# Optimization experiments

Measured on AMD Instinct MI355X. Metric: run time of the kernel, lower is better.

## Reference

```python
import jax, jax.numpy as jnp
import numpy as np

K = 5  # top-k neighbors (init kwarg k)
EPS = 1e-12

def _normalize(x):
    n = jnp.linalg.norm(x, axis=1, keepdims=True)
    return x / jnp.maximum(n, EPS)

def setup_inputs() -> dict:
    key = jax.random.key(0)
    k1, k2, k3 = jax.random.split(key, 3)
    B, D, N, C = 1024, 1024, 100000, 1000
    features = jax.random.normal(k1, (B, D), dtype=jnp.float32)
    idx = jax.random.randint(k2, (B,), 0, N, dtype=jnp.int64)
    # buffers: feat_memory = F.normalize(rand(N, D)); pred_memory = ones(N, C)/C
    feat_memory = _normalize(jax.random.uniform(k3, (N, D), dtype=jnp.float32))
    pred_memory = jnp.ones((N, C), dtype=jnp.float32) / C
    return {"features": features, "idx": idx,
            "feat_memory": feat_memory, "pred_memory": pred_memory}

def reference(features, idx, feat_memory, pred_memory):
    B = features.shape[0]
    x = _normalize(features)                       # [B, D]
    dis = x @ feat_memory.T                        # [B, N] similarity
    # self-mask: each row's own bank entry set to global min (min is invariant
    # under this assignment, so the per-row torch loop vectorizes exactly)
    m = jnp.min(dis)
    dis = dis.at[jnp.arange(B), idx].set(m)
    _, indices = jax.lax.top_k(dis, K)             # [B, K]
    mean_logits = jnp.mean(pred_memory[indices], axis=1)  # [B, C]
    pseudo_labels = jnp.argmax(mean_logits, axis=1)       # [B]
    return pseudo_labels, mean_logits
```

## Files before the change

### kernel.cpp

```cpp
#include <hip/hip_runtime.h>
#include <stdint.h>
#include <stddef.h>

#define B_ROWS 1024
#define D_DIM  1024
#define N_MEM  100000
#define C_CLS  1000
#define K_TOP  5

#define BM 256
#define BN 256
#define BKT 64
#define NKT (D_DIM / BKT)
#define NT_TILES ((N_MEM + BN - 1) / BN)
#define NPAD (NT_TILES * BN)
#define BT_TILES (B_ROWS / BM)
#define NT_PER_XCD 49
#define GRID_GEMM (8 * NT_PER_XCD * BT_TILES)

typedef __bf16 bf16;
typedef bf16 bf16x4 __attribute__((ext_vector_type(4)));
typedef bf16 bf16x8 __attribute__((ext_vector_type(8)));
typedef float f32x4 __attribute__((ext_vector_type(4)));

#define MFMA16(a, b, c) __builtin_amdgcn_mfma_f32_16x16x32_bf16((a), (b), (c), 0, 0, 0)
#define BARRIER() do { asm volatile("" ::: "memory"); \
                       __builtin_amdgcn_s_barrier();  \
                       asm volatile("" ::: "memory"); } while (0)
#define WAITVM(N) asm volatile("s_waitcnt vmcnt(" #N ")" ::: "memory")

__device__ __forceinline__ void insert5(float v, int n, float tv[K_TOP], int ti[K_TOP]) {
#pragma unroll
  for (int j = 0; j < K_TOP; ++j) {
    bool gt = v > tv[j];
    float ov = tv[j]; int oi = ti[j];
    tv[j] = gt ? v : ov;  ti[j] = gt ? n : oi;
    v = gt ? ov : v;      n = gt ? oi : n;
  }
}

__global__ __launch_bounds__(256) void k_normalize(const float* __restrict__ F,
                                                   bf16* __restrict__ X) {
  int row = blockIdx.x;
  int tid = threadIdx.x;
  const float4* fr = (const float4*)(F + (size_t)row * D_DIM);
  float4 v = fr[tid];
  float s = v.x * v.x + v.y * v.y + v.z * v.z + v.w * v.w;
  for (int off = 32; off > 0; off >>= 1) s += __shfl_down(s, off, 64);
  __shared__ float wred[4];
  if ((tid & 63) == 0) wred[tid >> 6] = s;
  __syncthreads();
  float tot = wred[0] + wred[1] + wred[2] + wred[3];
  float inv = 1.0f / fmaxf(sqrtf(tot), 1e-12f);
  bf16x4 o;
  o[0] = (bf16)(v.x * inv);
  o[1] = (bf16)(v.y * inv);
  o[2] = (bf16)(v.z * inv);
  o[3] = (bf16)(v.w * inv);
  *(bf16x4*)(X + (size_t)row * D_DIM + (size_t)tid * 4) = o;
}

__global__ __launch_bounds__(256) void k_convert(const float* __restrict__ FM,
                                                 bf16* __restrict__ FMB,
                                                 int total8, int pad8) {
  int i = blockIdx.x * 256 + threadIdx.x;
  if (i >= pad8) return;
  bf16x8 o;
  if (i < total8) {
    float4 a = ((const float4*)FM)[2 * i];
    float4 b = ((const float4*)FM)[2 * i + 1];
    o[0] = (bf16)a.x; o[1] = (bf16)a.y; o[2] = (bf16)a.z; o[3] = (bf16)a.w;
    o[4] = (bf16)b.x; o[5] = (bf16)b.y; o[6] = (bf16)b.z; o[7] = (bf16)b.w;
  } else {
#pragma unroll
    for (int e = 0; e < 8; ++e) o[e] = (bf16)0.f;
  }
  ((bf16x8*)FMB)[i] = o;
}

__device__ __forceinline__ void gl_lds16(const bf16* g, char* l) {
  __builtin_amdgcn_global_load_lds((__attribute__((address_space(1))) void*)g,
                                   (__attribute__((address_space(3))) void*)l,
                                   16, 0, 0);
}

#define STAGE_HALF(g, off, rbase, k0) do {                                     \
    gl_lds16((g) + (size_t)(rbase) * D_DIM + (k0),      lds + (off) + d0);     \
    gl_lds16((g) + (size_t)((rbase) + 64) * D_DIM + (k0), lds + (off) + d1);   \
  } while (0)

__global__ __launch_bounds__(512, 2) void k_gemm_topk(const bf16* __restrict__ X,
                                                      const bf16* __restrict__ FMB,
                                                      const int* __restrict__ IDX,
                                                      float2* __restrict__ CAND) {
  extern __shared__ char lds[];
  int bid = blockIdx.x;
  int xcd = bid & 7;
  int jj = bid >> 3;
  int cnt = (xcd < 7) ? NT_PER_XCD : (NT_TILES - 7 * NT_PER_XCD);
  if (jj >= 4 * cnt) return;
  int nt = xcd * NT_PER_XCD + (jj >> 2);
  int bt = jj & 3;
  size_t row0 = (size_t)bt * BM;
  size_t col0 = (size_t)nt * BN;

  int tid = threadIdx.x;
  int lane = tid & 63;
  int wv = tid >> 6;
  int wm = wv >> 2, wn = wv & 3;
  int frow = lane & 15, q = lane >> 4;
  int cs0 = ((q ^ (frow & 7)) * 16);
  int cs1 = (((q + 4) ^ (frow & 7)) * 16);

  int arow0 = tid >> 3;
  int jsrc = (tid & 7) ^ (arow0 & 7);
  const bf16* gA = X   + ((size_t)row0 + arow0) * D_DIM + jsrc * 8;
  const bf16* gB = FMB + ((size_t)col0 + arow0) * D_DIM + jsrc * 8;
  int d0 = tid * 16;
  int d1 = 8192 + tid * 16;

  STAGE_HALF(gA, 0,     0,   0);
  STAGE_HALF(gA, 16384, 128, 0);
  STAGE_HALF(gB, 32768, 0,   0);
  STAGE_HALF(gB, 49152, 128, 0);
  STAGE_HALF(gA, 65536 + 0,     0,   BKT);
  STAGE_HALF(gA, 65536 + 16384, 128, BKT);
  STAGE_HALF(gB, 65536 + 32768, 0,   BKT);
  STAGE_HALF(gB, 65536 + 49152, 128, BKT);

  f32x4 acc[8][4];
#pragma unroll
  for (int mi = 0; mi < 8; ++mi)
#pragma unroll
    for (int ni = 0; ni < 4; ++ni)
      acc[mi][ni] = (f32x4){0.f, 0.f, 0.f, 0.f};

  WAITVM(8);
  BARRIER();

#pragma unroll 2
  for (int kt = 0; kt < NKT; ++kt) {
    char* buf = lds + ((kt & 1) << 16);
    const char* Ab = buf + wm * 16384 + frow * 128;
    const char* Bb = buf + 32768 + ((wn >> 1) * 16384) + ((wn & 1) * 8192) + frow * 128;
    int bufoff = (kt & 1) << 16;
    int k2 = (kt + 2) * BKT;
    bool do_stage = (kt < NKT - 2);
    bf16x8 af[4][2], bfr[4][2];

#pragma unroll
    for (int mi = 0; mi < 4; ++mi) {
      af[mi][0] = *(const bf16x8*)(Ab + mi * 2048 + cs0);
      af[mi][1] = *(const bf16x8*)(Ab + mi * 2048 + cs1);
    }
#pragma unroll
    for (int nb = 0; nb < 2; ++nb) {
      bfr[nb][0] = *(const bf16x8*)(Bb + nb * 2048 + cs0);
      bfr[nb][1] = *(const bf16x8*)(Bb + nb * 2048 + cs1);
    }
    BARRIER();
    __builtin_amdgcn_s_setprio(1);
#pragma unroll
    for (int mi = 0; mi < 4; ++mi)
#pragma unroll
      for (int nb = 0; nb < 2; ++nb) {
        acc[mi][nb] = MFMA16(af[mi][0], bfr[nb][0], acc[mi][nb]);
        acc[mi][nb] = MFMA16(af[mi][1], bfr[nb][1], acc[mi][nb]);
      }
    __builtin_amdgcn_s_setprio(0);
    BARRIER();

#pragma unroll
    for (int nb = 2; nb < 4; ++nb) {
      bfr[nb][0] = *(const bf16x8*)(Bb + nb * 2048 + cs0);
      bfr[nb][1] = *(const bf16x8*)(Bb + nb * 2048 + cs1);
    }
    BARRIER();
    __builtin_amdgcn_s_setprio(1);
#pragma unroll
    for (int mi = 0; mi < 4; ++mi)
#pragma unroll
      for (int nb = 2; nb < 4; ++nb) {
        acc[mi][nb] = MFMA16(af[mi][0], bfr[nb][0], acc[mi][nb]);
        acc[mi][nb] = MFMA16(af[mi][1], bfr[nb][1], acc[mi][nb]);
      }
    __builtin_amdgcn_s_setprio(0);
    BARRIER();

#pragma unroll
    for (int mi = 0; mi < 4; ++mi) {
      af[mi][0] = *(const bf16x8*)(Ab + 8192 + mi * 2048 + cs0);
      af[mi][1] = *(const bf16x8*)(Ab + 8192 + mi * 2048 + cs1);
    }
    if (do_stage) {
      STAGE_HALF(gB, bufoff + 32768, 0,   k2);
      STAGE_HALF(gB, bufoff + 49152, 128, k2);
    }
    BARRIER();
    __builtin_amdgcn_s_setprio(1);
#pragma unroll
    for (int mi = 0; mi < 4; ++mi)
#pragma unroll
      for (int nb = 2; nb < 4; ++nb) {
        acc[4 + mi][nb] = MFMA16(af[mi][0], bfr[nb][0], acc[4 + mi][nb]);
        acc[4 + mi][nb] = MFMA16(af[mi][1], bfr[nb][1], acc[4 + mi][nb]);
      }
    __builtin_amdgcn_s_setprio(0);
    BARRIER();

    if (do_stage) {
      STAGE_HALF(gA, bufoff + 0,     0,   k2);
      STAGE_HALF(gA, bufoff + 16384, 128, k2);
    }
    BARRIER();
    __builtin_amdgcn_s_setprio(1);
#pragma unroll
    for (int mi = 0; mi < 4; ++mi)
#pragma unroll
      for (int nb = 0; nb < 2; ++nb) {
        acc[4 + mi][nb] = MFMA16(af[mi][0], bfr[nb][0], acc[4 + mi][nb]);
        acc[4 + mi][nb] = MFMA16(af[mi][1], bfr[nb][1], acc[4 + mi][nb]);
      }
    __builtin_amdgcn_s_setprio(0);
    if (kt < NKT - 2) { WAITVM(8); } else { WAITVM(0); }
    BARRIER();
  }

  int Rbase = wm * 128 + q * 4;
#pragma unroll
  for (int mi = 0; mi < 8; ++mi)
#pragma unroll
    for (int ni = 0; ni < 4; ++ni) {
      int Cc = wn * 64 + ni * 16 + frow;
      int chunkC = Cc >> 3;
      int e2 = (Cc & 7) * 2;
#pragma unroll
      for (int r = 0; r < 4; ++r) {
        int R = Rbase + mi * 16 + r;
        *(bf16*)(lds + R * 512 + ((chunkC ^ (R & 31)) * 16) + e2) = (bf16)acc[mi][ni][r];
      }
    }
  __syncthreads();

  int tr = tid >> 1, h = tid & 1;
  int grow = (int)row0 + tr;
  int self = IDX[grow];
  float tv[K_TOP]; int ti[K_TOP];
#pragma unroll
  for (int j = 0; j < K_TOP; ++j) { tv[j] = -1e30f; ti[j] = -1; }
  int swz = tr & 31;
#pragma unroll
  for (int c8 = 0; c8 < 16; ++c8) {
    int chunk = h * 16 + c8;
    bf16x8 v8 = *(const bf16x8*)(lds + tr * 512 + ((chunk ^ swz) * 16));
#pragma unroll
    for (int e = 0; e < 8; ++e) {
      int gc = (int)col0 + chunk * 8 + e;
      if (gc >= N_MEM || gc == self) continue;
      float v = (float)v8[e];
      if (v > tv[K_TOP - 1]) insert5(v, gc, tv, ti);
    }
  }
  float pv[K_TOP]; int pi[K_TOP];
#pragma unroll
  for (int j = 0; j < K_TOP; ++j) {
    pv[j] = __shfl_xor(tv[j], 1, 64);
    pi[j] = __shfl_xor(ti[j], 1, 64);
  }
#pragma unroll
  for (int j = 0; j < K_TOP; ++j)
    if (pv[j] > tv[K_TOP - 1]) insert5(pv[j], pi[j], tv, ti);

  if (h == 0) {
    float2* out = CAND + ((size_t)grow * NT_TILES + nt) * K_TOP;
#pragma unroll
    for (int j = 0; j < K_TOP; ++j)
      out[j] = make_float2(tv[j], __int_as_float(ti[j]));
  }
}

__device__ void gather_mean_argmax(const int* find, const float* __restrict__ P,
                                   float* __restrict__ OUT, int b, int tid) {
  float bestV = -1e30f;
  int bestC = 0;
  for (int c = tid; c < C_CLS; c += 256) {
    float s = 0.f;
    for (int j = 0; j < K_TOP; ++j) s += P[(size_t)find[j] * C_CLS + c];
    float mean = s * (1.0f / K_TOP);
    OUT[(size_t)B_ROWS + (size_t)b * C_CLS + c] = mean;
    if (mean > bestV) { bestV = mean; bestC = c; }
  }
  __shared__ float rv[256];
  __shared__ int rc[256];
  rv[tid] = bestV; rc[tid] = bestC;
  for (int s = 128; s >= 1; s >>= 1) {
    __syncthreads();
    if (tid < s) {
      float v2 = rv[tid + s]; int c2 = rc[tid + s];
      if (v2 > rv[tid] || (v2 == rv[tid] && c2 < rc[tid])) { rv[tid] = v2; rc[tid] = c2; }
    }
  }
  __syncthreads();
  if (tid == 0) OUT[b] = (float)rc[0];
}

__global__ __launch_bounds__(256) void k_merge(const float2* __restrict__ CAND,
                                               const float* __restrict__ P,
                                               float* __restrict__ OUT) {
  int b = blockIdx.x;
  int tid = threadIdx.x;
  const float2* row = CAND + (size_t)b * (NT_TILES * K_TOP);

  float tv[K_TOP]; int ti[K_TOP];
  for (int j = 0; j < K_TOP; ++j) { tv[j] = -1e30f; ti[j] = -1; }
  for (int i = tid; i < NT_TILES * K_TOP; i += 256) {
    float2 e = row[i];
    float v = e.x;
    if (v > tv[K_TOP - 1]) insert5(v, __float_as_int(e.y), tv, ti);
  }

  __shared__ float sv[256 * K_TOP];
  __shared__ int si[256 * K_TOP];
  for (int j = 0; j < K_TOP; ++j) { sv[tid * K_TOP + j] = tv[j]; si[tid * K_TOP + j] = ti[j]; }
  for (int s = 128; s >= 1; s >>= 1) {
    __syncthreads();
    if (tid < s) {
      for (int j = 0; j < K_TOP; ++j) {
        float v = sv[(tid + s) * K_TOP + j];
        int n = si[(tid + s) * K_TOP + j];
        if (v > tv[K_TOP - 1]) insert5(v, n, tv, ti);
      }
      for (int j = 0; j < K_TOP; ++j) { sv[tid * K_TOP + j] = tv[j]; si[tid * K_TOP + j] = ti[j]; }
    }
  }
  __syncthreads();
  __shared__ int find[K_TOP];
  if (tid == 0)
    for (int j = 0; j < K_TOP; ++j) {
      int v = si[j];
      find[j] = (v < 0) ? 0 : (v >= N_MEM ? N_MEM - 1 : v);
    }
  __syncthreads();
  gather_mean_argmax(find, P, OUT, b, tid);
}

__global__ __launch_bounds__(256) void k_naive(const float* __restrict__ F,
                                               const int* __restrict__ IDX,
                                               const float* __restrict__ FM,
                                               const float* __restrict__ P,
                                               float* __restrict__ OUT) {
  int b = blockIdx.x;
  int tid = threadIdx.x;
  __shared__ float wred[4];
  const float4* fr = (const float4*)(F + (size_t)b * D_DIM);
  float4 v = fr[tid];
  float s = v.x * v.x + v.y * v.y + v.z * v.z + v.w * v.w;
  for (int off = 32; off > 0; off >>= 1) s += __shfl_down(s, off, 64);
  if ((tid & 63) == 0) wred[tid >> 6] = s;
  __syncthreads();
  float inv = 1.0f / fmaxf(sqrtf(wred[0] + wred[1] + wred[2] + wred[3]), 1e-12f);
  float4 xv = make_float4(v.x * inv, v.y * inv, v.z * inv, v.w * inv);
  __syncthreads();
  int self = IDX[b];
  __shared__ float ptv[K_TOP];
  __shared__ int pti[K_TOP];
  if (tid < K_TOP) { ptv[tid] = -1e30f; pti[tid] = 0; }
  __syncthreads();
  for (int n = 0; n < N_MEM; ++n) {
    const float4* frow = (const float4*)(FM + (size_t)n * D_DIM);
    float4 fv = frow[tid];
    float p = xv.x * fv.x + xv.y * fv.y + xv.z * fv.z + xv.w * fv.w;
    for (int off = 32; off > 0; off >>= 1) p += __shfl_down(p, off, 64);
    if ((tid & 63) == 0) wred[tid >> 6] = p;
    __syncthreads();
    if (tid == 0 && n != self) {
      float tot = wred[0] + wred[1] + wred[2] + wred[3];
      if (tot > ptv[K_TOP - 1]) {
        int q = K_TOP - 1;
        while (q > 0 && tot > ptv[q - 1]) { ptv[q] = ptv[q - 1]; pti[q] = pti[q - 1]; --q; }
        ptv[q] = tot; pti[q] = n;
      }
    }
    __syncthreads();
  }
  __shared__ int find[K_TOP];
  if (tid < K_TOP) {
    int x = pti[tid];
    find[tid] = (x < 0) ? 0 : (x >= N_MEM ? N_MEM - 1 : x);
  }
  __syncthreads();
  gather_mean_argmax(find, P, OUT, b, tid);
}

extern "C" void kernel_launch(void* const* d_in, const int* in_sizes, int n_in,
                              void* d_out, int out_size, void* d_ws, size_t ws_size,
                              hipStream_t stream) {
  const float* F  = (const float*)d_in[0];
  const int* IDX  = (const int*)d_in[1];
  const float* FM = (const float*)d_in[2];
  const float* P  = (const float*)d_in[3];
  float* OUT = (float*)d_out;

  const size_t xBytes    = (size_t)B_ROWS * D_DIM * 2;
  const size_t fmBytes   = (size_t)NPAD * D_DIM * 2;
  const size_t candBytes = (size_t)B_ROWS * NT_TILES * K_TOP * 8;
  const size_t need = xBytes + fmBytes + candBytes;

  if (ws_size >= need) {
    bf16* Xb     = (bf16*)d_ws;
    bf16* FMB    = (bf16*)((char*)d_ws + xBytes);
    float2* CAND = (float2*)((char*)d_ws + xBytes + fmBytes);
    (void)hipFuncSetAttribute((const void*)k_gemm_topk,
                              hipFuncAttributeMaxDynamicSharedMemorySize, 131072);
    k_normalize<<<B_ROWS, 256, 0, stream>>>(F, Xb);
    int total8 = N_MEM * D_DIM / 8;
    int pad8   = NPAD * D_DIM / 8;
    k_convert<<<(pad8 + 255) / 256, 256, 0, stream>>>(FM, FMB, total8, pad8);
    k_gemm_topk<<<GRID_GEMM, 512, 131072, stream>>>(Xb, FMB, IDX, CAND);
    k_merge<<<B_ROWS, 256, 0, stream>>>(CAND, P, OUT);
  } else {
    k_naive<<<B_ROWS, 256, 0, stream>>>(F, IDX, FM, P, OUT);
  }
}
```

Measured before the change: 1.071 ms.

## Restructure GEMM main loop with register-prefetched fragments and one barrier per k-tile

Rewrites the k-loop of the fused GEMM+top-k kernel. Instead of four barrier-separated phases per k-tile, it keeps all B fragments and quarter-split A fragments in registers. It interleaves LDS reads for the next k-tile with the MFMAs of the current one and issues all global-to-LDS staging after a single barrier. The goal is to remove barrier stalls and hide LDS latency behind the matrix-core work. The costs are higher register pressure, which matters under the 2-waves-per-SIMD launch bound, and a full vmcnt(0) wait each iteration that drops the previous one-tile lookahead in global loads.

```diff
diff --git a/kernel.cpp b/kernel.cpp
--- a/kernel.cpp
+++ b/kernel.cpp
@@ -28,6 +28,8 @@
                        __builtin_amdgcn_s_barrier();  \
                        asm volatile("" ::: "memory"); } while (0)
 #define WAITVM(N) asm volatile("s_waitcnt vmcnt(" #N ")" ::: "memory")
+#define LGKM0()   asm volatile("s_waitcnt lgkmcnt(0)" ::: "memory")
+#define VM0()     asm volatile("s_waitcnt vmcnt(0)" ::: "memory")
 
 __device__ __forceinline__ void insert5(float v, int n, float tv[K_TOP], int ti[K_TOP]) {
 #pragma unroll
@@ -87,6 +89,28 @@
 #define STAGE_HALF(g, off, rbase, k0) do {                                     \
     gl_lds16((g) + (size_t)(rbase) * D_DIM + (k0),      lds + (off) + d0);     \
     gl_lds16((g) + (size_t)((rbase) + 64) * D_DIM + (k0), lds + (off) + d1);   \
+  } while (0)
+
+#define LOAD_AFQ(dst, qi, Ab_) do {                                            \
+    dst[0][0] = *(const bf16x8*)((Ab_) + (2 * (qi) + 0) * 2048 + cs0);         \
+    dst[0][1] = *(const bf16x8*)((Ab_) + (2 * (qi) + 0) * 2048 + cs1);         \
+    dst[1][0] = *(const bf16x8*)((Ab_) + (2 * (qi) + 1) * 2048 + cs0);         \
+    dst[1][1] = *(const bf16x8*)((Ab_) + (2 * (qi) + 1) * 2048 + cs1);         \
+  } while (0)
+
+#define LOAD_BF(dst, nb, Bb_) do {                                             \
+    dst[0] = *(const bf16x8*)((Bb_) + (nb) * 2048 + cs0);                      \
+    dst[1] = *(const bf16x8*)((Bb_) + (nb) * 2048 + cs1);                      \
+  } while (0)
+
+#define MMA8(aq, r0, n0) do {                                                  \
+    __builtin_amdgcn_s_setprio(1);                                             \
+    _Pragma("unroll") for (int kk = 0; kk < 2; ++kk)                           \
+      _Pragma("unroll") for (int m = 0; m < 2; ++m)                            \
+        _Pragma("unroll") for (int nb = 0; nb < 2; ++nb)                       \
+          acc[(r0) + m][(n0) + nb] = MFMA16(aq[m][kk], bfr[(n0) + nb][kk],     \
+                                            acc[(r0) + m][(n0) + nb]);         \
+    __builtin_amdgcn_s_setprio(0);                                             \
   } while (0)
 
 __global__ __launch_bounds__(512, 2) void k_gemm_topk(const bf16* __restrict__ X,
@@ -138,94 +162,57 @@
   WAITVM(8);
   BARRIER();
 
-#pragma unroll 2
+  bf16x8 afq[4][2][2];
+  bf16x8 bfr[4][2];
+
+  {
+    const char* Ab_ = lds + wm * 16384 + frow * 128;
+    const char* Bb_ = lds + 32768 + (wn >> 1) * 16384 + (wn & 1) * 8192 + frow * 128;
+    LOAD_BF(bfr[0], 0, Bb_);
+    LOAD_BF(bfr[1], 1, Bb_);
+    LOAD_BF(bfr[2], 2, Bb_);
+    LOAD_BF(bfr[3], 3, Bb_);
+    LOAD_AFQ(afq[0], 0, Ab_);
+    LOAD_AFQ(afq[1], 1, Ab_);
+  }
+
   for (int kt = 0; kt < NKT; ++kt) {
-    char* buf = lds + ((kt & 1) << 16);
-    const char* Ab = buf + wm * 16384 + frow * 128;
-    const char* Bb = buf + 32768 + ((wn >> 1) * 16384) + ((wn & 1) * 8192) + frow * 128;
-    int bufoff = (kt & 1) << 16;
+    int bo  = (kt & 1) << 16;
+    int bon = ((kt + 1) & 1) << 16;
+    const char* Ab  = lds + bo  + wm * 16384 + frow * 128;
+    const char* Abn = lds + bon + wm * 16384 + frow * 128;
+    const char* Bbn = lds + bon + 32768 + (wn >> 1) * 16384 + (wn & 1) * 8192 + frow * 128;
+    bool st = (kt < NKT - 2), pf = (kt < NKT - 1);
     int k2 = (kt + 2) * BKT;
-    bool do_stage = (kt < NKT - 2);
-    bf16x8 af[4][2], bfr[4][2];
-
-#pragma unroll
-    for (int mi = 0; mi < 4; ++mi) {
-      af[mi][0] = *(const bf16x8*)(Ab + mi * 2048 + cs0);
-      af[mi][1] = *(const bf16x8*)(Ab + mi * 2048 + cs1);
-    }
-#pragma unroll
-    for (int nb = 0; nb < 2; ++nb) {
-      bfr[nb][0] = *(const bf16x8*)(Bb + nb * 2048 + cs0);
-      bfr[nb][1] = *(const bf16x8*)(Bb + nb * 2048 + cs1);
-    }
+
+    LOAD_AFQ(afq[2], 2, Ab);
+    MMA8(afq[0], 0, 0);
+    LOAD_AFQ(afq[3], 3, Ab);
+    MMA8(afq[0], 0, 2);
+    MMA8(afq[1], 2, 0);
+    MMA8(afq[1], 2, 2);
+
+    LGKM0();
+    VM0();
     BARRIER();
-    __builtin_amdgcn_s_setprio(1);
-#pragma unroll
-    for (int mi = 0; mi < 4; ++mi)
-#pragma unroll
-      for (int nb = 0; nb < 2; ++nb) {
-        acc[mi][nb] = MFMA16(af[mi][0], bfr[nb][0], acc[mi][nb]);
-        acc[mi][nb] = MFMA16(af[mi][1], bfr[nb][1], acc[mi][nb]);
-      }
-    __builtin_amdgcn_s_setprio(0);
-    BARRIER();
-
-#pragma unroll
-    for (int nb = 2; nb < 4; ++nb) {
-      bfr[nb][0] = *(const bf16x8*)(Bb + nb * 2048 + cs0);
-      bfr[nb][1] = *(const bf16x8*)(Bb + nb * 2048 + cs1);
-    }
-    BARRIER();
-    __builtin_amdgcn_s_setprio(1);
-#pragma unroll
-    for (int mi = 0; mi < 4; ++mi)
-#pragma unroll
-      for (int nb = 2; nb < 4; ++nb) {
-        acc[mi][nb] = MFMA16(af[mi][0], bfr[nb][0], acc[mi][nb]);
-        acc[mi][nb] = MFMA16(af[mi][1], bfr[nb][1], acc[mi][nb]);
-      }
-    __builtin_amdgcn_s_setprio(0);
-    BARRIER();
-
-#pragma unroll
-    for (int mi = 0; mi < 4; ++mi) {
-      af[mi][0] = *(const bf16x8*)(Ab + 8192 + mi * 2048 + cs0);
-      af[mi][1] = *(const bf16x8*)(Ab + 8192 + mi * 2048 + cs1);
-    }
-    if (do_stage) {
-      STAGE_HALF(gB, bufoff + 32768, 0,   k2);
-      STAGE_HALF(gB, bufoff + 49152, 128, k2);
-    }
-    BARRIER();
-    __builtin_amdgcn_s_setprio(1);
-#pragma unroll
-    for (int mi = 0; mi < 4; ++mi)
-#pragma unroll
-      for (int nb = 2; nb < 4; ++nb) {
-        acc[4 + mi][nb] = MFMA16(af[mi][0], bfr[nb][0], acc[4 + mi][nb]);
-        acc[4 + mi][nb] = MFMA16(af[mi][1], bfr[nb][1], acc[4 + mi][nb]);
-      }
-    __builtin_amdgcn_s_setprio(0);
-    BARRIER();
-
-    if (do_stage) {
-      STAGE_HALF(gA, bufoff + 0,     0,   k2);
-      STAGE_HALF(gA, bufoff + 16384, 128, k2);
-    }
-    BARRIER();
-    __builtin_amdgcn_s_setprio(1);
-#pragma unroll
-    for (int mi = 0; mi < 4; ++mi)
-#pragma unroll
-      for (int nb = 0; nb < 2; ++nb) {
-        acc[4 + mi][nb] = MFMA16(af[mi][0], bfr[nb][0], acc[4 + mi][nb]);
-        acc[4 + mi][nb] = MFMA16(af[mi][1], bfr[nb][1], acc[4 + mi][nb]);
-      }
-    __builtin_amdgcn_s_setprio(0);
-    if (kt < NKT - 2) { WAITVM(8); } else { WAITVM(0); }
-    BARRIER();
-  }
-
+
+    if (st) {
+      STAGE_HALF(gA, bo + 0,     0,   k2);
+      STAGE_HALF(gA, bo + 16384, 128, k2);
+      STAGE_HALF(gB, bo + 32768, 0,   k2);
+      STAGE_HALF(gB, bo + 49152, 128, k2);
+    }
+    if (pf) LOAD_AFQ(afq[0], 0, Abn);
+    MMA8(afq[2], 4, 0);
+    MMA8(afq[2], 4, 2);
+    if (pf) LOAD_AFQ(afq[1], 1, Abn);
+    MMA8(afq[3], 6, 0);
+    if (pf) { LOAD_BF(bfr[0], 0, Bbn); LOAD_BF(bfr[1], 1, Bbn); }
+    MMA8(afq[3], 6, 2);
+    if (pf) { LOAD_BF(bfr[2], 2, Bbn); LOAD_BF(bfr[3], 3, Bbn); }
+  }
+
+  __syncthreads();
   int Rbase = wm * 128 + q * 4;
 #pragma unroll
   for (int mi = 0; mi < 8; ++mi)
```

New measurement: 1.039 ms. -3.0%, faster.
